# Kernel tuning notes

Hardware: AMD Instinct MI355X
Metric: run time of the kernel (lower is better)

## Reference

```python
import jax, jax.numpy as jnp
import numpy as np

N_INIT = jnp.array([17.047, 14.099, 3.625], dtype=jnp.float32)
CA_INIT = jnp.array([16.967, 12.784, 4.338], dtype=jnp.float32)
C_INIT = jnp.array([15.685, 12.755, 5.133], dtype=jnp.float32)


def _unit(x):
    return x / (jnp.linalg.norm(x, axis=-1, keepdims=True) + 1e-8)


def _place_dihedral(a, b, c, bond_angle, bond_length, torsion):
    # a,b,c: [B,3]; bond_angle/bond_length/torsion: [B]
    ab = b - a
    bc = _unit(c - b)
    cr = jnp.cross(ab, bc)
    crn = jnp.linalg.norm(cr, axis=-1, keepdims=True)
    n_main = _unit(cr)
    # collinear fallback (per-element; almost never triggers for real angles)
    perp = jnp.zeros_like(bc).at[..., 0].set(1.0)
    ct = jnp.cross(bc, perp)
    ctn = jnp.linalg.norm(ct, axis=-1, keepdims=True)
    perp2 = jnp.where(ctn < 1e-6, jnp.zeros_like(bc).at[..., 1].set(1.0), perp)
    n_fb = _unit(jnp.cross(bc, perp2))
    n = jnp.where(crn < 1e-6, n_fb, n_main)
    nbc = jnp.cross(n, bc)
    m = jnp.stack([bc, nbc, n], axis=-1)  # [B,3,3]
    d_local = jnp.stack([
        -bond_length * jnp.cos(bond_angle),
        bond_length * jnp.cos(torsion) * jnp.sin(bond_angle),
        bond_length * jnp.sin(torsion) * jnp.sin(bond_angle),
    ], axis=-1)  # [B,3]
    d = jnp.einsum('bij,bj->bi', m, d_local)
    return d + c


def _nerf_build(phi, psi, omega, bond_lengths, bond_angles):
    B, L = phi.shape
    init = jnp.broadcast_to(jnp.stack([N_INIT, CA_INIT, C_INIT]), (B, 3, 3))
    # per-step params, leading axis = residue index i in [0, L-2]
    xs = (
        psi[:, :L - 1].T,                 # psi_i
        omega[:, :L - 1].T,               # omega_i
        phi[:, 1:].T,                     # phi_{i+1}
        bond_lengths[:, :L - 1, 2].T,     # C-N length
        bond_lengths[:, :L - 1, 0].T,     # N-CA length
        bond_lengths[:, :L - 1, 1].T,     # CA-C length
        bond_angles[:, :L - 1, 1].T,      # CA-C-N angle
        bond_angles[:, :L - 1, 2].T,      # C-N-CA angle
        bond_angles[:, :L - 1, 0].T,      # N-CA-C angle
    )

    def step(prev, x):
        psi_i, omega_i, phi_i, len_cn, len_nca, len_cac, ang_cacn, ang_cnca, ang_ncac = x
        a, b, c = prev[:, 0], prev[:, 1], prev[:, 2]
        n = _place_dihedral(a, b, c, ang_cacn, len_cn, psi_i)
        ca = _place_dihedral(b, c, n, ang_cnca, len_nca, omega_i)
        cc = _place_dihedral(c, n, ca, ang_ncac, len_cac, phi_i)
        new = jnp.stack([n, ca, cc], axis=1)  # [B,3,3]
        return new, new

    _, outs = jax.lax.scan(step, init, xs)  # [L-1,B,3,3]
    rest = outs.transpose(1, 0, 2, 3).reshape(B, 3 * (L - 1), 3)
    return jnp.concatenate([init, rest], axis=1)  # [B, 3L, 3]


def setup_inputs() -> dict:
    key = jax.random.key(0)
    k0, k1, k2, k3, k4 = jax.random.split(key, 5)
    B, L = 4096, 512
    phi = jax.random.normal(k0, (B, L), dtype=jnp.float32)
    psi = jax.random.normal(k1, (B, L), dtype=jnp.float32)
    omega = jax.random.normal(k2, (B, L), dtype=jnp.float32)
    # realistic positive bond lengths (~1.0-1.5 A) and bond angles (~1.5-2.3 rad)
    bond_lengths = 1.0 + 0.5 * jax.random.uniform(k3, (B, L, 3), dtype=jnp.float32)
    bond_angles = 1.5 + 0.8 * jax.random.uniform(k4, (B, L, 3), dtype=jnp.float32)
    return {"phi": phi, "psi": psi, "omega": omega,
            "bond_lengths": bond_lengths, "bond_angles": bond_angles}


def reference(phi, psi, omega, bond_lengths, bond_angles):
    return _nerf_build(phi, psi, omega, bond_lengths, bond_angles)
```

## Files before the change

kernel.cpp:

```cpp
#include <hip/hip_runtime.h>
#include <math.h>


#define LCH 512

struct Xf { float r[9]; float t[3]; };

__device__ __forceinline__ Xf xf_compose(const Xf& A, const Xf& B) {
  Xf C;
#pragma unroll
  for (int i = 0; i < 3; ++i) {
    float a0 = A.r[3*i+0], a1 = A.r[3*i+1], a2 = A.r[3*i+2];
    C.r[3*i+0] = a0*B.r[0] + a1*B.r[3] + a2*B.r[6];
    C.r[3*i+1] = a0*B.r[1] + a1*B.r[4] + a2*B.r[7];
    C.r[3*i+2] = a0*B.r[2] + a1*B.r[5] + a2*B.r[8];
    C.t[i]     = a0*B.t[0] + a1*B.t[1] + a2*B.t[2] + A.t[i];
  }
  return C;
}

__device__ __forceinline__ void xf_step(Xf& P, float theta, float len, float tau) {
  float st, ct, sx, cx;
  __sincosf(theta, &st, &ct);
  __sincosf(tau, &sx, &cx);
  float ux = -ct, uy = cx*st, uz = sx*st;
  float v0 = -st, v1 = -ct*cx, v2 = -ct*sx;
  float c00 = P.r[0]*ux + P.r[1]*uy + P.r[2]*uz;
  float c10 = P.r[3]*ux + P.r[4]*uy + P.r[5]*uz;
  float c20 = P.r[6]*ux + P.r[7]*uy + P.r[8]*uz;
  float c01 = P.r[0]*v0 + P.r[1]*v1 + P.r[2]*v2;
  float c11 = P.r[3]*v0 + P.r[4]*v1 + P.r[5]*v2;
  float c21 = P.r[6]*v0 + P.r[7]*v1 + P.r[8]*v2;
  float c02 = P.r[2]*cx - P.r[1]*sx;
  float c12 = P.r[5]*cx - P.r[4]*sx;
  float c22 = P.r[8]*cx - P.r[7]*sx;
  P.t[0] += len*c00; P.t[1] += len*c10; P.t[2] += len*c20;
  P.r[0]=c00; P.r[1]=c01; P.r[2]=c02;
  P.r[3]=c10; P.r[4]=c11; P.r[5]=c12;
  P.r[6]=c20; P.r[7]=c21; P.r[8]=c22;
}

__device__ __forceinline__ void xf_set_delta(Xf& P, float theta, float len, float tau) {
  float st, ct, sx, cx;
  __sincosf(theta, &st, &ct);
  __sincosf(tau, &sx, &cx);
  float ux = -ct, uy = cx*st, uz = sx*st;
  P.r[0]=ux; P.r[1]=-st;    P.r[2]=0.f;
  P.r[3]=uy; P.r[4]=-ct*cx; P.r[5]=-sx;
  P.r[6]=uz; P.r[7]=-ct*sx; P.r[8]=cx;
  P.t[0]=len*ux; P.t[1]=len*uy; P.t[2]=len*uz;
}

__device__ __forceinline__ void xf_identity(Xf& A) {
  A.r[0]=1.f; A.r[1]=0.f; A.r[2]=0.f;
  A.r[3]=0.f; A.r[4]=1.f; A.r[5]=0.f;
  A.r[6]=0.f; A.r[7]=0.f; A.r[8]=1.f;
  A.t[0]=0.f; A.t[1]=0.f; A.t[2]=0.f;
}

__device__ __forceinline__ Xf xf_shfl_up(const Xf& P, int d) {
  Xf O;
#pragma unroll
  for (int i = 0; i < 9; ++i) O.r[i] = __shfl_up(P.r[i], d, 64);
#pragma unroll
  for (int i = 0; i < 3; ++i) O.t[i] = __shfl_up(P.t[i], d, 64);
  return O;
}

#define REP(f) (A.r[3*((f)%3)+0]*sx[(f)/3] + A.r[3*((f)%3)+1]*sy[(f)/3] \
              + A.r[3*((f)%3)+2]*sz[(f)/3] + A.t[(f)%3])

__global__ __launch_bounds__(256, 2) void nerf_r9_kernel(
    const float* __restrict__ g_phi, const float* __restrict__ g_psi,
    const float* __restrict__ g_omg, const float* __restrict__ g_bl,
    const float* __restrict__ g_ba, float* __restrict__ g_out, int nchain)
{
  const int lane  = threadIdx.x & 63;
  const int wave  = threadIdx.x >> 6;
  const int chain = blockIdx.x * 4 + wave;
  if (chain >= nchain) return;

  const float* phir = g_phi + (size_t)chain * LCH;
  const float* psir = g_psi + (size_t)chain * LCH;
  const float* omgr = g_omg + (size_t)chain * LCH;
  const float* blr  = g_bl  + (size_t)chain * (LCH*3);
  const float* bar  = g_ba  + (size_t)chain * (LCH*3);

  const int j8  = 8 * lane;
  const int b24 = 24 * lane;

  float PS[8], OM[8], PH[8], BL[24], BA[24];
  {
    float  e0 = psir[j8 ? j8 - 1 : 0];
    float4 v0 = *(const float4*)(psir + j8);
    float2 v1 = *(const float2*)(psir + j8 + 4);
    float  e7 = psir[j8 + 6];
    PS[0]=e0; PS[1]=v0.x; PS[2]=v0.y; PS[3]=v0.z; PS[4]=v0.w; PS[5]=v1.x; PS[6]=v1.y; PS[7]=e7;
  }
  {
    float  e0 = omgr[j8 ? j8 - 1 : 0];
    float4 v0 = *(const float4*)(omgr + j8);
    float2 v1 = *(const float2*)(omgr + j8 + 4);
    float  e7 = omgr[j8 + 6];
    OM[0]=e0; OM[1]=v0.x; OM[2]=v0.y; OM[3]=v0.z; OM[4]=v0.w; OM[5]=v1.x; OM[6]=v1.y; OM[7]=e7;
  }
  {
    float4 v0 = *(const float4*)(phir + j8);
    float4 v1 = *(const float4*)(phir + j8 + 4);
    PH[0]=v0.x; PH[1]=v0.y; PH[2]=v0.z; PH[3]=v0.w;
    PH[4]=v1.x; PH[5]=v1.y; PH[6]=v1.z; PH[7]=v1.w;
  }
  {
    float  e0  = blr[b24 >= 3 ? b24 - 3 : 0];
    float2 e12 = *(const float2*)(blr + (b24 >= 2 ? b24 - 2 : 0));
    float4 w0 = *(const float4*)(blr + b24);
    float4 w1 = *(const float4*)(blr + b24 + 4);
    float4 w2 = *(const float4*)(blr + b24 + 8);
    float4 w3 = *(const float4*)(blr + b24 + 12);
    float4 w4 = *(const float4*)(blr + b24 + 16);
    float  e23 = blr[b24 + 20];
    BL[0]=e0;   BL[1]=e12.x; BL[2]=e12.y;
    BL[3]=w0.x; BL[4]=w0.y;  BL[5]=w0.z;  BL[6]=w0.w;
    BL[7]=w1.x; BL[8]=w1.y;  BL[9]=w1.z;  BL[10]=w1.w;
    BL[11]=w2.x; BL[12]=w2.y; BL[13]=w2.z; BL[14]=w2.w;
    BL[15]=w3.x; BL[16]=w3.y; BL[17]=w3.z; BL[18]=w3.w;
    BL[19]=w4.x; BL[20]=w4.y; BL[21]=w4.z; BL[22]=w4.w;
    BL[23]=e23;
  }
  {
    float  e0  = bar[b24 >= 3 ? b24 - 3 : 0];
    float2 e12 = *(const float2*)(bar + (b24 >= 2 ? b24 - 2 : 0));
    float4 w0 = *(const float4*)(bar + b24);
    float4 w1 = *(const float4*)(bar + b24 + 4);
    float4 w2 = *(const float4*)(bar + b24 + 8);
    float4 w3 = *(const float4*)(bar + b24 + 12);
    float4 w4 = *(const float4*)(bar + b24 + 16);
    float  e23 = bar[b24 + 20];
    BA[0]=e0;   BA[1]=e12.x; BA[2]=e12.y;
    BA[3]=w0.x; BA[4]=w0.y;  BA[5]=w0.z;  BA[6]=w0.w;
    BA[7]=w1.x; BA[8]=w1.y;  BA[9]=w1.z;  BA[10]=w1.w;
    BA[11]=w2.x; BA[12]=w2.y; BA[13]=w2.z; BA[14]=w2.w;
    BA[15]=w3.x; BA[16]=w3.y; BA[17]=w3.z; BA[18]=w3.w;
    BA[19]=w4.x; BA[20]=w4.y; BA[21]=w4.z; BA[22]=w4.w;
    BA[23]=e23;
  }

  Xf P;
  float sx[24], sy[24], sz[24];
#pragma unroll
  for (int k = 0; k < 24; ++k) {
    const int m = k / 3, a = k - 3*m;
    float th, ln, ta;
    if (a == 0)      { th = BA[3*m+1]; ln = BL[3*m+2]; ta = PS[m]; }
    else if (a == 1) { th = BA[3*m+2]; ln = BL[3*m+0]; ta = OM[m]; }
    else             { th = BA[3*m+0]; ln = BL[3*m+1]; ta = PH[m]; }
    if (k == 0) xf_set_delta(P, th, ln, ta);
    else        xf_step(P, th, ln, ta);
    sx[k] = P.t[0]; sy[k] = P.t[1]; sz[k] = P.t[2];
    if (k == 2 && lane == 0) xf_identity(P);
  }

#pragma unroll
  for (int d = 1; d < 64; d <<= 1) {
    Xf O = xf_shfl_up(P, d);
    if (lane >= d) P = xf_compose(O, P);
  }
  Xf E = xf_shfl_up(P, 1);

  Xf A;
  {
    const float ax=17.047f, ay=14.099f, az=3.625f;
    const float bx_=16.967f, by_=12.784f, bz_=4.338f;
    const float cx_=15.685f, cy_=12.755f, cz_=5.133f;
    float abx=bx_-ax, aby=by_-ay, abz=bz_-az;
    float vx=cx_-bx_, vy=cy_-by_, vz=cz_-bz_;
    float vn = sqrtf(vx*vx+vy*vy+vz*vz) + 1e-8f;
    vx/=vn; vy/=vn; vz/=vn;
    float crx = aby*vz - abz*vy;
    float cry = abz*vx - abx*vz;
    float crz = abx*vy - aby*vx;
    float cn = sqrtf(crx*crx+cry*cry+crz*crz) + 1e-8f;
    float nx=crx/cn, ny=cry/cn, nz=crz/cn;
    float mx = ny*vz - nz*vy;
    float my = nz*vx - nx*vz;
    float mz = nx*vy - ny*vx;
    A.r[0]=vx; A.r[1]=mx; A.r[2]=nx;
    A.r[3]=vy; A.r[4]=my; A.r[5]=ny;
    A.r[6]=vz; A.r[7]=mz; A.r[8]=nz;
    A.t[0]=cx_; A.t[1]=cy_; A.t[2]=cz_;
  }
  if (lane > 0) A = xf_compose(A, E);

  float* orow = g_out + (size_t)chain * 4608 + 72 * lane;
#pragma unroll
  for (int q = 0; q < 18; ++q) {
    float4 v;
    v.x = REP(4*q + 0);
    v.y = REP(4*q + 1);
    v.z = REP(4*q + 2);
    v.w = REP(4*q + 3);
    *(float4*)(orow + 4*q) = v;
  }
  if (lane == 0) {
    float4 i0; i0.x=17.047f; i0.y=14.099f; i0.z=3.625f;  i0.w=16.967f;
    float4 i1; i1.x=12.784f; i1.y=4.338f;  i1.z=15.685f; i1.w=12.755f;
    *(float4*)(orow + 0) = i0;
    *(float4*)(orow + 4) = i1;
    orow[8] = 5.133f;
  }
}

extern "C" void kernel_launch(void* const* d_in, const int* in_sizes, int n_in,
                              void* d_out, int out_size, void* d_ws, size_t ws_size,
                              hipStream_t stream) {
  const float* phi = (const float*)d_in[0];
  const float* psi = (const float*)d_in[1];
  const float* omg = (const float*)d_in[2];
  const float* bl  = (const float*)d_in[3];
  const float* ba  = (const float*)d_in[4];
  float* out = (float*)d_out;
  const int B = in_sizes[0] / LCH;
  const int blocks = (B + 3) / 4;
  hipLaunchKernelGGL(nerf_r9_kernel, dim3(blocks), dim3(256), 0, stream,
                     phi, psi, omg, bl, ba, out, B);
}
```

Baseline: 153.4 us.

## Split each chain across two waves with shared-memory cross-wave prefix combine

Each chain is now handled by a 128-thread block (two waves) instead of one wave, so each thread covers 4 residues instead of 8. The wave-level transform scan is extended with a shared-memory handoff: wave 0's total transform is stored and composed into wave 1's base frame after a __syncthreads. This doubles the thread count and lowers per-thread register use and serial work, which should raise occupancy and latency hiding. The cost is an extra block barrier, a second shuffle scan per chain, and the loss of the chain-count bounds check.

```diff
diff --git a/kernel.cpp b/kernel.cpp
--- a/kernel.cpp
+++ b/kernel.cpp
@@ -70,15 +70,17 @@
 #define REP(f) (A.r[3*((f)%3)+0]*sx[(f)/3] + A.r[3*((f)%3)+1]*sy[(f)/3] \
               + A.r[3*((f)%3)+2]*sz[(f)/3] + A.t[(f)%3])
 
-__global__ __launch_bounds__(256, 2) void nerf_r9_kernel(
+__global__ __launch_bounds__(128) void nerf_r10_kernel(
     const float* __restrict__ g_phi, const float* __restrict__ g_psi,
     const float* __restrict__ g_omg, const float* __restrict__ g_bl,
-    const float* __restrict__ g_ba, float* __restrict__ g_out, int nchain)
+    const float* __restrict__ g_ba, float* __restrict__ g_out)
 {
-  const int lane  = threadIdx.x & 63;
-  const int wave  = threadIdx.x >> 6;
-  const int chain = blockIdx.x * 4 + wave;
-  if (chain >= nchain) return;
+  __shared__ float s_tot[12];
+
+  const int t    = threadIdx.x;
+  const int lane = t & 63;
+  const int wave = t >> 6;
+  const int chain = blockIdx.x;
 
   const float* phir = g_phi + (size_t)chain * LCH;
   const float* psir = g_psi + (size_t)chain * LCH;
@@ -86,69 +88,51 @@
   const float* blr  = g_bl  + (size_t)chain * (LCH*3);
   const float* bar  = g_ba  + (size_t)chain * (LCH*3);
 
-  const int j8  = 8 * lane;
-  const int b24 = 24 * lane;
-
-  float PS[8], OM[8], PH[8], BL[24], BA[24];
-  {
-    float  e0 = psir[j8 ? j8 - 1 : 0];
-    float4 v0 = *(const float4*)(psir + j8);
-    float2 v1 = *(const float2*)(psir + j8 + 4);
-    float  e7 = psir[j8 + 6];
-    PS[0]=e0; PS[1]=v0.x; PS[2]=v0.y; PS[3]=v0.z; PS[4]=v0.w; PS[5]=v1.x; PS[6]=v1.y; PS[7]=e7;
-  }
-  {
-    float  e0 = omgr[j8 ? j8 - 1 : 0];
-    float4 v0 = *(const float4*)(omgr + j8);
-    float2 v1 = *(const float2*)(omgr + j8 + 4);
-    float  e7 = omgr[j8 + 6];
-    OM[0]=e0; OM[1]=v0.x; OM[2]=v0.y; OM[3]=v0.z; OM[4]=v0.w; OM[5]=v1.x; OM[6]=v1.y; OM[7]=e7;
-  }
-  {
-    float4 v0 = *(const float4*)(phir + j8);
-    float4 v1 = *(const float4*)(phir + j8 + 4);
-    PH[0]=v0.x; PH[1]=v0.y; PH[2]=v0.z; PH[3]=v0.w;
-    PH[4]=v1.x; PH[5]=v1.y; PH[6]=v1.z; PH[7]=v1.w;
-  }
-  {
-    float  e0  = blr[b24 >= 3 ? b24 - 3 : 0];
-    float2 e12 = *(const float2*)(blr + (b24 >= 2 ? b24 - 2 : 0));
-    float4 w0 = *(const float4*)(blr + b24);
-    float4 w1 = *(const float4*)(blr + b24 + 4);
-    float4 w2 = *(const float4*)(blr + b24 + 8);
-    float4 w3 = *(const float4*)(blr + b24 + 12);
-    float4 w4 = *(const float4*)(blr + b24 + 16);
-    float  e23 = blr[b24 + 20];
+  const int j4  = 4 * t;
+  const int b12 = 12 * t;
+
+  float PS[4], OM[4], PH[4], BL[12], BA[12];
+  {
+    float  e0 = psir[j4 ? j4 - 1 : 0];
+    float4 v  = *(const float4*)(psir + j4);
+    PS[0]=e0; PS[1]=v.x; PS[2]=v.y; PS[3]=v.z;
+  }
+  {
+    float  e0 = omgr[j4 ? j4 - 1 : 0];
+    float4 v  = *(const float4*)(omgr + j4);
+    OM[0]=e0; OM[1]=v.x; OM[2]=v.y; OM[3]=v.z;
+  }
+  {
+    float4 v = *(const float4*)(phir + j4);
+    PH[0]=v.x; PH[1]=v.y; PH[2]=v.z; PH[3]=v.w;
+  }
+  {
+    float  e0  = blr[b12 >= 3 ? b12 - 3 : 0];
+    float2 e12 = *(const float2*)(blr + (b12 >= 2 ? b12 - 2 : 0));
+    float4 w0  = *(const float4*)(blr + b12);
+    float4 w1  = *(const float4*)(blr + b12 + 4);
+    float  e8  = blr[b12 + 8];
     BL[0]=e0;   BL[1]=e12.x; BL[2]=e12.y;
     BL[3]=w0.x; BL[4]=w0.y;  BL[5]=w0.z;  BL[6]=w0.w;
     BL[7]=w1.x; BL[8]=w1.y;  BL[9]=w1.z;  BL[10]=w1.w;
-    BL[11]=w2.x; BL[12]=w2.y; BL[13]=w2.z; BL[14]=w2.w;
-    BL[15]=w3.x; BL[16]=w3.y; BL[17]=w3.z; BL[18]=w3.w;
-    BL[19]=w4.x; BL[20]=w4.y; BL[21]=w4.z; BL[22]=w4.w;
-    BL[23]=e23;
-  }
-  {
-    float  e0  = bar[b24 >= 3 ? b24 - 3 : 0];
-    float2 e12 = *(const float2*)(bar + (b24 >= 2 ? b24 - 2 : 0));
-    float4 w0 = *(const float4*)(bar + b24);
-    float4 w1 = *(const float4*)(bar + b24 + 4);
-    float4 w2 = *(const float4*)(bar + b24 + 8);
-    float4 w3 = *(const float4*)(bar + b24 + 12);
-    float4 w4 = *(const float4*)(bar + b24 + 16);
-    float  e23 = bar[b24 + 20];
+    BL[11]=e8;
+  }
+  {
+    float  e0  = bar[b12 >= 3 ? b12 - 3 : 0];
+    float2 e12 = *(const float2*)(bar + (b12 >= 2 ? b12 - 2 : 0));
+    float4 w0  = *(const float4*)(bar + b12);
+    float4 w1  = *(const float4*)(bar + b12 + 4);
+    float  e8  = bar[b12 + 8];
     BA[0]=e0;   BA[1]=e12.x; BA[2]=e12.y;
     BA[3]=w0.x; BA[4]=w0.y;  BA[5]=w0.z;  BA[6]=w0.w;
     BA[7]=w1.x; BA[8]=w1.y;  BA[9]=w1.z;  BA[10]=w1.w;
-    BA[11]=w2.x; BA[12]=w2.y; BA[13]=w2.z; BA[14]=w2.w;
-    BA[15]=w3.x; BA[16]=w3.y; BA[17]=w3.z; BA[18]=w3.w;
-    BA[19]=w4.x; BA[20]=w4.y; BA[21]=w4.z; BA[22]=w4.w;
-    BA[23]=e23;
+    BA[11]=e8;
   }
 
   Xf P;
-  float sx[24], sy[24], sz[24];
-#pragma unroll
-  for (int k = 0; k < 24; ++k) {
+  float sx[12], sy[12], sz[12];
+#pragma unroll
+  for (int k = 0; k < 12; ++k) {
     const int m = k / 3, a = k - 3*m;
     float th, ln, ta;
     if (a == 0)      { th = BA[3*m+1]; ln = BL[3*m+2]; ta = PS[m]; }
@@ -157,7 +141,7 @@
     if (k == 0) xf_set_delta(P, th, ln, ta);
     else        xf_step(P, th, ln, ta);
     sx[k] = P.t[0]; sy[k] = P.t[1]; sz[k] = P.t[2];
-    if (k == 2 && lane == 0) xf_identity(P);
+    if (k == 2 && t == 0) xf_identity(P);
   }
 
 #pragma unroll
@@ -165,7 +149,15 @@
     Xf O = xf_shfl_up(P, d);
     if (lane >= d) P = xf_compose(O, P);
   }
+
+  if (wave == 0 && lane == 63) {
+#pragma unroll
+    for (int i = 0; i < 9; ++i) s_tot[i] = P.r[i];
+#pragma unroll
+    for (int i = 0; i < 3; ++i) s_tot[9+i] = P.t[i];
+  }
   Xf E = xf_shfl_up(P, 1);
+  __syncthreads();
 
   Xf A;
   {
@@ -189,11 +181,19 @@
     A.r[6]=vz; A.r[7]=mz; A.r[8]=nz;
     A.t[0]=cx_; A.t[1]=cy_; A.t[2]=cz_;
   }
+  if (wave == 1) {
+    Xf T;
+#pragma unroll
+    for (int i = 0; i < 9; ++i) T.r[i] = s_tot[i];
+#pragma unroll
+    for (int i = 0; i < 3; ++i) T.t[i] = s_tot[9+i];
+    A = xf_compose(A, T);
+  }
   if (lane > 0) A = xf_compose(A, E);
 
-  float* orow = g_out + (size_t)chain * 4608 + 72 * lane;
-#pragma unroll
-  for (int q = 0; q < 18; ++q) {
+  float* orow = g_out + (size_t)chain * 4608 + 36 * t;
+#pragma unroll
+  for (int q = 0; q < 9; ++q) {
     float4 v;
     v.x = REP(4*q + 0);
     v.y = REP(4*q + 1);
@@ -201,7 +201,7 @@
     v.w = REP(4*q + 3);
     *(float4*)(orow + 4*q) = v;
   }
-  if (lane == 0) {
+  if (t == 0) {
     float4 i0; i0.x=17.047f; i0.y=14.099f; i0.z=3.625f;  i0.w=16.967f;
     float4 i1; i1.x=12.784f; i1.y=4.338f;  i1.z=15.685f; i1.w=12.755f;
     *(float4*)(orow + 0) = i0;
@@ -220,7 +220,6 @@
   const float* ba  = (const float*)d_in[4];
   float* out = (float*)d_out;
   const int B = in_sizes[0] / LCH;
-  const int blocks = (B + 3) / 4;
-  hipLaunchKernelGGL(nerf_r9_kernel, dim3(blocks), dim3(256), 0, stream,
-                     phi, psi, omg, bl, ba, out, B);
-}
+  hipLaunchKernelGGL(nerf_r10_kernel, dim3(B), dim3(128), 0, stream,
+                     phi, psi, omg, bl, ba, out);
+}
```

New measurement: 156.6 us. 2.1% more time.
